# Optimization experiments

Hardware: AMD Instinct MI355X
Metric: run time of the kernel (lower is better)

## Reference

```python
import jax, jax.numpy as jnp
import numpy as np

D = 256      # linear_dim
H = 8        # heads
B, S = 4, 2048


def setup_inputs() -> dict:
    key = jax.random.key(0)
    ks = jax.random.split(key, 9)
    scale = 1.0 / np.sqrt(D)
    x = jax.random.normal(ks[0], (B, S, D), dtype=jnp.float32)
    # per-head Linear weights stacked: [H, out, in] (torch Linear layout)
    Wq = jax.random.normal(ks[1], (H, D, D), dtype=jnp.float32) * scale
    bq = jax.random.normal(ks[2], (H, D), dtype=jnp.float32) * scale
    Wk = jax.random.normal(ks[3], (H, D, D), dtype=jnp.float32) * scale
    bk = jax.random.normal(ks[4], (H, D), dtype=jnp.float32) * scale
    Wv = jax.random.normal(ks[5], (H, D, D), dtype=jnp.float32) * scale
    bv = jax.random.normal(ks[6], (H, D), dtype=jnp.float32) * scale
    Wo = jax.random.normal(ks[7], (D, H * D), dtype=jnp.float32) * (1.0 / np.sqrt(H * D))
    bo = jax.random.normal(ks[8], (D,), dtype=jnp.float32) * scale
    return {"x": x, "Wq": Wq, "bq": bq, "Wk": Wk, "bk": bk,
            "Wv": Wv, "bv": bv, "Wo": Wo, "bo": bo}


def reference(x, Wq, bq, Wk, bk, Wv, bv, Wo, bo):
    # Batched per-head projections (torch Linear: y = x @ W.T + b)
    Q = jnp.einsum('bsd,hed->bhse', x, Wq) + bq[None, :, None, :]  # [B,H,S,D]
    K = jnp.einsum('bsd,hed->bhse', x, Wk) + bk[None, :, None, :]
    V = jnp.einsum('bsd,hed->bhse', x, Wv) + bv[None, :, None, :]
    scores = jnp.einsum('bhse,bhte->bhst', Q, K) / jnp.sqrt(jnp.float32(D))  # [B,H,Sq,Sk]
    # FAITHFUL quirk: original softmaxes over dim=1 of [B,S,S] -> the QUERY axis.
    attn = jax.nn.softmax(scores, axis=2)
    Z = jnp.einsum('bhst,bhte->bhse', attn, V)       # [B,H,S,D]
    Z = jnp.transpose(Z, (0, 2, 1, 3)).reshape(B, S, H * D)  # concat heads (head-major order matches torch.cat)
    return jnp.einsum('bsf,of->bso', Z, Wo) + bo
```

## Files before the change

### kernel.cpp

```cpp
#include <hip/hip_runtime.h>
#include <hip/hip_bf16.h>

#define DEV __device__ __forceinline__

typedef __bf16 bf16x8 __attribute__((ext_vector_type(8)));
typedef float f32x4 __attribute__((ext_vector_type(4)));

DEV f32x4 mfma16(bf16x8 a, bf16x8 b, f32x4 c) {
  return __builtin_amdgcn_mfma_f32_16x16x32_bf16(a, b, c, 0, 0, 0);
}

DEV ushort f2bf(float f) {
  union { __hip_bfloat16 h; ushort u; } cv;
  cv.h = __float2bfloat16(f);
  return cv.u;
}
DEV float bf2f(ushort u) {
  union { float f; unsigned v; } cv; cv.v = ((unsigned)u) << 16; return cv.f;
}


__global__ __launch_bounds__(256) void convert_all(
    const float* __restrict__ x, const float* __restrict__ wq,
    const float* __restrict__ wk, const float* __restrict__ wv,
    const float* __restrict__ wo, ushort* __restrict__ dst)
{
  size_t i = ((size_t)blockIdx.x * 256 + threadIdx.x) * 4;
  const float* src; size_t off;
  if (i < (size_t)2097152) { src = x; off = i; }
  else {
    size_t j = i - 2097152;
    unsigned wsel = (unsigned)(j >> 19);
    off = j & 524287;
    src = wsel == 0 ? wq : wsel == 1 ? wk : wsel == 2 ? wv : wo;
  }
  float4 v = *(const float4*)(src + off);
  ushort4 o;
  o.x = f2bf(v.x); o.y = f2bf(v.y); o.z = f2bf(v.z); o.w = f2bf(v.w);
  *(ushort4*)(dst + i) = o;
}

template<int BM, int BN, int EPI>
__global__ __launch_bounds__(256, 2) void gemm_nt(
    const ushort* __restrict__ A,
    const ushort* __restrict__ W0, const ushort* __restrict__ W1, const ushort* __restrict__ W2,
    int K,
    const float* __restrict__ b0, const float* __restrict__ b1, const float* __restrict__ b2,
    ushort* __restrict__ Qo, ushort* __restrict__ Ko, ushort* __restrict__ Vo,
    float* __restrict__ fo)
{
  constexpr int WM = BM / 2, WN = BN / 2, MF = WM / 16, NF = WN / 16;
  constexpr int CA = BM / 64, CB = BN / 64;
  const int n0 = blockIdx.x * BN, m0 = blockIdx.y * BM;
  const int tid = threadIdx.x, lane = tid & 63;
  const int wm = (tid >> 7) & 1, wn = (tid >> 6) & 1;

  __shared__ ushort As[BM * 40];
  __shared__ ushort Bs[BN * 40];

  const ushort* Bt;
  if (EPI == 0) {
    int p = n0 >> 11;
    Bt = (p == 0 ? W0 : p == 1 ? W1 : W2) + (size_t)(n0 & 2047) * K;
  } else {
    Bt = W0 + (size_t)n0 * K;
  }

  f32x4 acc[MF][NF];
#pragma unroll
  for (int m = 0; m < MF; m++)
#pragma unroll
    for (int n = 0; n < NF; n++) acc[m][n] = (f32x4){0.f, 0.f, 0.f, 0.f};

  for (int k0 = 0; k0 < K; k0 += 32) {
#pragma unroll
    for (int i = 0; i < CA; i++) {
      int ci = tid * CA + i; int r = ci >> 2, c = ci & 3;
      *(uint4*)&As[r * 40 + c * 8] = *(const uint4*)&A[(size_t)(m0 + r) * K + k0 + c * 8];
    }
#pragma unroll
    for (int i = 0; i < CB; i++) {
      int ci = tid * CB + i; int r = ci >> 2, c = ci & 3;
      *(uint4*)&Bs[r * 40 + c * 8] = *(const uint4*)&Bt[(size_t)r * K + k0 + c * 8];
    }
    __syncthreads();
    bf16x8 af[MF], bfr[NF];
#pragma unroll
    for (int m = 0; m < MF; m++)
      af[m] = *(const bf16x8*)&As[(wm * WM + m * 16 + (lane & 15)) * 40 + ((lane >> 4) << 3)];
#pragma unroll
    for (int n = 0; n < NF; n++)
      bfr[n] = *(const bf16x8*)&Bs[(wn * WN + n * 16 + (lane & 15)) * 40 + ((lane >> 4) << 3)];
#pragma unroll
    for (int m = 0; m < MF; m++)
#pragma unroll
      for (int n = 0; n < NF; n++) acc[m][n] = mfma16(af[m], bfr[n], acc[m][n]);
    __syncthreads();
  }

  if (EPI == 0) {
    const int p = n0 >> 11;
    const float* bias = (p == 0 ? b0 : p == 1 ? b1 : b2);
    const float scl = (p == 0 ? 0.0625f : 1.0f);
#pragma unroll
    for (int m = 0; m < MF; m++)
#pragma unroll
      for (int n = 0; n < NF; n++)
#pragma unroll
        for (int r = 0; r < 4; r++) {
          int row = m0 + wm * WM + m * 16 + ((lane >> 4) << 2) + r;
          int col = n0 + wn * WN + n * 16 + (lane & 15);
          int ce = col & 2047;
          float v = (acc[m][n][r] + bias[ce]) * scl;
          int b = row >> 11, s = row & 2047, h = ce >> 8, e = ce & 255;
          int bh = b * 8 + h;
          if (p == 0) {
            Qo[((size_t)(bh * 2048 + s) << 8) + e] = f2bf(v);
          } else if (p == 1) {
            int ee = ((((e >> 3) ^ (s & 7)) & 31) << 3) | (e & 7);
            Ko[((size_t)(bh * 2048 + s) << 8) + ee] = f2bf(v);
          } else {
            Vo[(((size_t)bh * 64 + (s >> 5)) << 13) + e * 32 + (s & 31)] = f2bf(v);
          }
        }
  } else {
#pragma unroll
    for (int m = 0; m < MF; m++)
#pragma unroll
      for (int n = 0; n < NF; n++)
#pragma unroll
        for (int r = 0; r < 4; r++) {
          int row = m0 + wm * WM + m * 16 + ((lane >> 4) << 2) + r;
          int col = n0 + wn * WN + n * 16 + (lane & 15);
          fo[(size_t)row * 256 + col] = acc[m][n][r] + b0[col];
        }
  }
}

__global__ __launch_bounds__(256, 4) void attn_p0(
    const ushort* __restrict__ Qb, const ushort* __restrict__ Kb,
    float* __restrict__ lpart)
{
  const int bid = blockIdx.x;
  const int swz = (bid & 7) * 128 + (bid >> 3);
  const int bh = swz >> 5, stile = swz & 31;
  const int s0 = stile * 64;
  const int tid = threadIdx.x, lane = tid & 63, w = tid >> 6;
  const int g = lane >> 4, r15 = lane & 15;

  __shared__ ushort Ks[2][8192];

  bf16x8 q[8];
  {
    const ushort* qrow = &Qb[((size_t)bh * 2048 + s0 + w * 16 + r15) * 256 + g * 8];
#pragma unroll
    for (int kk = 0; kk < 8; kk++) q[kk] = *(const bf16x8*)&qrow[kk * 32];
  }

  const ushort* Ktile = Kb + ((size_t)bh << 19);

  uint4 st[4];
#pragma unroll
  for (int i = 0; i < 4; ++i)
    st[i] = *(const uint4*)&Ktile[(size_t)(i * 256 + tid) * 8];
#pragma unroll
  for (int i = 0; i < 4; ++i)
    *(uint4*)&Ks[0][(i * 256 + tid) * 8] = st[i];

  int cur = 0;
  for (int it = 0; it < 64; ++it) {
    __syncthreads();
    if (it < 63) {
#pragma unroll
      for (int i = 0; i < 4; ++i)
        st[i] = *(const uint4*)&Ktile[(size_t)(it + 1) * 8192 + (i * 256 + tid) * 8];
    }
    f32x4 gg[2];
    gg[0] = (f32x4){0.f, 0.f, 0.f, 0.f};
    gg[1] = (f32x4){0.f, 0.f, 0.f, 0.f};
    const ushort* ks = &Ks[cur][0];
#pragma unroll
    for (int n = 0; n < 2; ++n)
#pragma unroll
      for (int kk = 0; kk < 8; ++kk) {
        bf16x8 kb = *(const bf16x8*)&ks[(n * 16 + r15) * 256 + (((kk * 4 + g) ^ (r15 & 7)) << 3)];
        gg[n] = mfma16(q[kk], kb, gg[n]);
      }
#pragma unroll
    for (int n = 0; n < 2; ++n) {
      float sn = __expf(gg[n][0]) + __expf(gg[n][1]) + __expf(gg[n][2]) + __expf(gg[n][3]);
      sn += __shfl_xor(sn, 16);
      sn += __shfl_xor(sn, 32);
      if (g == 0)
        lpart[((size_t)((stile * 4 + w) * 32 + bh) << 11) + it * 32 + n * 16 + r15] = sn;
    }
    if (it < 63) {
#pragma unroll
      for (int i = 0; i < 4; ++i)
        *(uint4*)&Ks[cur ^ 1][(i * 256 + tid) * 8] = st[i];
    }
    cur ^= 1;
  }
}

__global__ __launch_bounds__(256, 2) void attn_p1(
    const ushort* __restrict__ Qb, const ushort* __restrict__ Kb,
    const ushort* __restrict__ Vt, ushort* __restrict__ Zb)
{
  const int bid = blockIdx.x;
  const int swz = (bid & 7) * 64 + (bid >> 3);
  const int bh = swz >> 4, stile = swz & 15;
  const int s0 = stile * 128;
  const int tid = threadIdx.x, lane = tid & 63, w = tid >> 6;
  const int g = lane >> 4, r15 = lane & 15;

  __shared__ __align__(16) ushort Ks[2][8192];
  __shared__ __align__(16) ushort Ps[2][5120];

  bf16x8 q[2][8];
#pragma unroll
  for (int h = 0; h < 2; ++h) {
    const ushort* qrow = &Qb[((size_t)bh * 2048 + s0 + w * 32 + h * 16 + r15) * 256 + g * 8];
#pragma unroll
    for (int kk = 0; kk < 8; kk++) q[h][kk] = *(const bf16x8*)&qrow[kk * 32];
  }

  const ushort* Ktile = Kb + ((size_t)bh << 19);
  const ushort* Vtile = Vt + ((size_t)bh << 19);

  f32x4 acc[8][4];
#pragma unroll
  for (int m = 0; m < 8; m++)
#pragma unroll
    for (int n = 0; n < 4; n++) acc[m][n] = (f32x4){0.f, 0.f, 0.f, 0.f};

  {
    uint4 p0[4];
#pragma unroll
    for (int i = 0; i < 4; ++i)
      p0[i] = *(const uint4*)&Ktile[(size_t)(i * 256 + tid) * 8];
#pragma unroll
    for (int i = 0; i < 4; ++i)
      *(uint4*)&Ks[0][(i * 256 + tid) * 8] = p0[i];
  }
  __syncthreads();

  for (int it = 0; it < 64; ++it) {
    const int cur = it & 1;
    bf16x8 vb[4];
#pragma unroll
    for (int n = 0; n < 4; ++n)
      vb[n] = *(const bf16x8*)&Vtile[(size_t)it * 8192 + (w * 64 + n * 16 + r15) * 32 + g * 8];
    uint4 st[4];
    if (it < 63) {
#pragma unroll
      for (int i = 0; i < 4; ++i)
        st[i] = *(const uint4*)&Ktile[(size_t)(it + 1) * 8192 + (i * 256 + tid) * 8];
    }

#pragma unroll
    for (int h = 0; h < 2; ++h) {
      f32x4 gg[2];
      gg[0] = (f32x4){0.f, 0.f, 0.f, 0.f};
      gg[1] = (f32x4){0.f, 0.f, 0.f, 0.f};
#pragma unroll
      for (int n = 0; n < 2; ++n)
#pragma unroll
        for (int kk = 0; kk < 8; ++kk) {
          bf16x8 kb = *(const bf16x8*)&Ks[cur][(n * 16 + r15) * 256 + (((kk * 4 + g) ^ (r15 & 7)) << 3)];
          gg[n] = mfma16(q[h][kk], kb, gg[n]);
        }
#pragma unroll
      for (int n = 0; n < 2; ++n)
#pragma unroll
        for (int rr = 0; rr < 4; ++rr)
          Ps[cur][(w * 32 + h * 16 + g * 4 + rr) * 40 + n * 16 + r15] = f2bf(__expf(gg[n][rr]));
    }

    if (it < 63) {
#pragma unroll
      for (int i = 0; i < 4; ++i)
        *(uint4*)&Ks[cur ^ 1][(i * 256 + tid) * 8] = st[i];
    }

    __syncthreads();

#pragma unroll
    for (int mh = 0; mh < 2; ++mh) {
      bf16x8 pa[4];
#pragma unroll
      for (int m = 0; m < 4; ++m)
        pa[m] = *(const bf16x8*)&Ps[cur][((mh * 4 + m) * 16 + r15) * 40 + g * 8];
#pragma unroll
      for (int n = 0; n < 4; ++n)
#pragma unroll
        for (int m = 0; m < 4; ++m)
          acc[mh * 4 + m][n] = mfma16(pa[m], vb[n], acc[mh * 4 + m][n]);
    }
  }

  const int b = bh >> 3, h = bh & 7;
#pragma unroll
  for (int m = 0; m < 8; m++)
#pragma unroll
    for (int n = 0; n < 4; n++)
#pragma unroll
      for (int rr = 0; rr < 4; rr++) {
        int sl = m * 16 + g * 4 + rr;
        int el = w * 64 + n * 16 + r15;
        Zb[((size_t)(b * 2048 + s0 + sl)) * 2048 + h * 256 + el] = f2bf(acc[m][n][rr]);
      }
}

__global__ __launch_bounds__(256) void vscale(
    ushort* __restrict__ Vt, const float* __restrict__ lp)
{
  const int tt = blockIdx.x, bh = blockIdx.y, tid = threadIdx.x;
  const int t = tid & 31, pg = tid >> 5;
  __shared__ float red[256];
  __shared__ float cinv[32];
  float s = 0.f;
  for (int p = pg * 16; p < pg * 16 + 16; ++p)
    s += lp[(((size_t)p * 32 + bh) << 11) + tt * 32 + t];
  red[tid] = s;
  __syncthreads();
  if (tid < 32) {
    float tot = 0.f;
#pragma unroll
    for (int i = 0; i < 8; ++i) tot += red[tid + i * 32];
    cinv[tid] = 1.0f / tot;
  }
  __syncthreads();
  size_t base = (((size_t)bh * 64 + tt) << 13) + (size_t)tid * 32;
  ushort buf[32];
#pragma unroll
  for (int i = 0; i < 4; ++i) *(uint4*)&buf[i * 8] = *(const uint4*)&Vt[base + i * 8];
#pragma unroll
  for (int j = 0; j < 32; ++j) buf[j] = f2bf(bf2f(buf[j]) * cinv[j]);
#pragma unroll
  for (int i = 0; i < 4; ++i) *(uint4*)&Vt[base + i * 8] = *(const uint4*)&buf[i * 8];
}

extern "C" void kernel_launch(void* const* d_in, const int* in_sizes, int n_in,
                              void* d_out, int out_size, void* d_ws, size_t ws_size,
                              hipStream_t stream) {
  const float* x  = (const float*)d_in[0];
  const float* Wq = (const float*)d_in[1];
  const float* bq = (const float*)d_in[2];
  const float* Wk = (const float*)d_in[3];
  const float* bk = (const float*)d_in[4];
  const float* Wv = (const float*)d_in[5];
  const float* bv = (const float*)d_in[6];
  const float* Wo = (const float*)d_in[7];
  const float* bo = (const float*)d_in[8];

  if (ws_size < (size_t)176160768) return;

  char* ws = (char*)d_ws;
  ushort* bfb = (ushort*)ws;
  ushort* xb  = bfb;
  ushort* wqb = bfb + 2097152;
  ushort* wkb = bfb + 2621440;
  ushort* wvb = bfb + 3145728;
  ushort* wob = bfb + 3670016;
  ushort* Qb = (ushort*)(ws + 8388608);
  ushort* Kb = (ushort*)(ws + 41943040);
  ushort* Vt = (ushort*)(ws + 75497472);
  ushort* Zb = (ushort*)(ws + 109051904);
  float*  lp = (float*)(ws + 142606336);
  float* out = (float*)d_out;

  convert_all<<<4096, 256, 0, stream>>>(x, Wq, Wk, Wv, Wo, bfb);
  gemm_nt<128, 128, 0><<<dim3(48, 64), 256, 0, stream>>>(
      xb, wqb, wkb, wvb, 256, bq, bk, bv, Qb, Kb, Vt, nullptr);
  attn_p0<<<1024, 256, 0, stream>>>(Qb, Kb, lp);
  vscale<<<dim3(64, 32), 256, 0, stream>>>(Vt, lp);
  attn_p1<<<512, 256, 0, stream>>>(Qb, Kb, Vt, Zb);
  gemm_nt<64, 64, 1><<<dim3(4, 128), 256, 0, stream>>>(
      Zb, wob, wob, wob, 2048, bo, bo, bo, nullptr, nullptr, nullptr, out);
}
```

Measured before the change: 380.7 us.

## Double query rows per block in attn_p0 and split key range across blocks

Each attn_p0 block now covers 128 query rows, two 16-row groups per wave, and only half of the key tiles. Every K fragment loaded from LDS is reused for two MFMAs, which halves the number of K tile loads per query row. The partial column-sum buffer now holds 64 partitions instead of 128, and vscale reduces over fewer partials. The block count stays the same, but each wave carries more registers for Q and the accumulators.

```diff
diff --git a/kernel.cpp b/kernel.cpp
--- a/kernel.cpp
+++ b/kernel.cpp
@@ -143,58 +143,64 @@
 {
   const int bid = blockIdx.x;
   const int swz = (bid & 7) * 128 + (bid >> 3);
-  const int bh = swz >> 5, stile = swz & 31;
-  const int s0 = stile * 64;
+  const int bh = swz >> 5, stile = (swz >> 1) & 15, half = swz & 1;
+  const int s0 = stile * 128;
   const int tid = threadIdx.x, lane = tid & 63, w = tid >> 6;
   const int g = lane >> 4, r15 = lane & 15;
 
   __shared__ ushort Ks[2][8192];
 
-  bf16x8 q[8];
-  {
-    const ushort* qrow = &Qb[((size_t)bh * 2048 + s0 + w * 16 + r15) * 256 + g * 8];
-#pragma unroll
-    for (int kk = 0; kk < 8; kk++) q[kk] = *(const bf16x8*)&qrow[kk * 32];
+  bf16x8 q[2][8];
+#pragma unroll
+  for (int h = 0; h < 2; ++h) {
+    const ushort* qrow = &Qb[((size_t)bh * 2048 + s0 + w * 32 + h * 16 + r15) * 256 + g * 8];
+#pragma unroll
+    for (int kk = 0; kk < 8; kk++) q[h][kk] = *(const bf16x8*)&qrow[kk * 32];
   }
 
   const ushort* Ktile = Kb + ((size_t)bh << 19);
+  const int it0 = half * 32, it1 = it0 + 32;
 
   uint4 st[4];
 #pragma unroll
   for (int i = 0; i < 4; ++i)
-    st[i] = *(const uint4*)&Ktile[(size_t)(i * 256 + tid) * 8];
+    st[i] = *(const uint4*)&Ktile[(size_t)it0 * 8192 + (i * 256 + tid) * 8];
 #pragma unroll
   for (int i = 0; i < 4; ++i)
     *(uint4*)&Ks[0][(i * 256 + tid) * 8] = st[i];
 
   int cur = 0;
-  for (int it = 0; it < 64; ++it) {
+  for (int it = it0; it < it1; ++it) {
     __syncthreads();
-    if (it < 63) {
+    if (it < it1 - 1) {
 #pragma unroll
       for (int i = 0; i < 4; ++i)
         st[i] = *(const uint4*)&Ktile[(size_t)(it + 1) * 8192 + (i * 256 + tid) * 8];
     }
-    f32x4 gg[2];
-    gg[0] = (f32x4){0.f, 0.f, 0.f, 0.f};
-    gg[1] = (f32x4){0.f, 0.f, 0.f, 0.f};
+    f32x4 gg[2][2];
+#pragma unroll
+    for (int h = 0; h < 2; ++h)
+#pragma unroll
+      for (int n = 0; n < 2; ++n) gg[h][n] = (f32x4){0.f, 0.f, 0.f, 0.f};
     const ushort* ks = &Ks[cur][0];
 #pragma unroll
     for (int n = 0; n < 2; ++n)
 #pragma unroll
       for (int kk = 0; kk < 8; ++kk) {
         bf16x8 kb = *(const bf16x8*)&ks[(n * 16 + r15) * 256 + (((kk * 4 + g) ^ (r15 & 7)) << 3)];
-        gg[n] = mfma16(q[kk], kb, gg[n]);
+        gg[0][n] = mfma16(q[0][kk], kb, gg[0][n]);
+        gg[1][n] = mfma16(q[1][kk], kb, gg[1][n]);
       }
 #pragma unroll
     for (int n = 0; n < 2; ++n) {
-      float sn = __expf(gg[n][0]) + __expf(gg[n][1]) + __expf(gg[n][2]) + __expf(gg[n][3]);
+      float sn = __expf(gg[0][n][0]) + __expf(gg[0][n][1]) + __expf(gg[0][n][2]) + __expf(gg[0][n][3])
+               + __expf(gg[1][n][0]) + __expf(gg[1][n][1]) + __expf(gg[1][n][2]) + __expf(gg[1][n][3]);
       sn += __shfl_xor(sn, 16);
       sn += __shfl_xor(sn, 32);
       if (g == 0)
         lpart[((size_t)((stile * 4 + w) * 32 + bh) << 11) + it * 32 + n * 16 + r15] = sn;
     }
-    if (it < 63) {
+    if (it < it1 - 1) {
 #pragma unroll
       for (int i = 0; i < 4; ++i)
         *(uint4*)&Ks[cur ^ 1][(i * 256 + tid) * 8] = st[i];
@@ -320,7 +326,7 @@
   __shared__ float red[256];
   __shared__ float cinv[32];
   float s = 0.f;
-  for (int p = pg * 16; p < pg * 16 + 16; ++p)
+  for (int p = pg * 8; p < pg * 8 + 8; ++p)
     s += lp[(((size_t)p * 32 + bh) << 11) + tt * 32 + t];
   red[tid] = s;
   __syncthreads();
```

Result: slower. 415.5 us (+9.1%).
